# Optimization experiments

Measured on AMD Instinct MI355X. Metric: run time of the kernel, lower is better.

The kernel has to match this reference:

```python
import jax, jax.numpy as jnp
import numpy as np

N, E, F_IN, H, G, C = 50000, 600000, 128, 128, 500, 10


def _lin(k, fi, fo):
    # Glorot-ish scaled init for a [fi, fo] weight
    return (jax.random.normal(k, (fi, fo), jnp.float32) / np.float32(np.sqrt(fi)))


def setup_inputs() -> dict:
    key = jax.random.key(0)
    ks = jax.random.split(key, 16)
    x = jax.random.normal(ks[0], (N, F_IN), jnp.float32)
    edge_index = jax.random.randint(ks[1], (2, E), 0, N, dtype=jnp.int32)
    batch = jnp.sort(jax.random.randint(ks[2], (N,), 0, G, dtype=jnp.int32))
    return {
        "x": x, "edge_index": edge_index, "batch": batch,
        # SAGEConv i: out = mean_aggr @ Wl + bl + x @ Wr  (PyG default: mean aggr, root weight, bias on lin_l)
        "Wl1": _lin(ks[3], F_IN, H), "bl1": jnp.zeros((H,), jnp.float32), "Wr1": _lin(ks[4], F_IN, H),
        "Wl2": _lin(ks[5], H, H),    "bl2": jnp.zeros((H,), jnp.float32), "Wr2": _lin(ks[6], H, H),
        "Wl3": _lin(ks[7], H, H),    "bl3": jnp.zeros((H,), jnp.float32), "Wr3": _lin(ks[8], H, H),
        "W4": _lin(ks[9], H, 64), "b4": jnp.zeros((64,), jnp.float32),
        "W5": _lin(ks[10], 64, C), "b5": jnp.zeros((C,), jnp.float32),
    }


def _segment_mean(vals, ids, num_segments):
    s = jax.ops.segment_sum(vals, ids, num_segments=num_segments)
    cnt = jax.ops.segment_sum(jnp.ones((vals.shape[0], 1), vals.dtype), ids, num_segments=num_segments)
    return s / jnp.maximum(cnt, 1.0)


def _sage_conv(x, src, dst, Wl, bl, Wr):
    # gather source features along edges, mean-aggregate at destinations
    aggr = _segment_mean(x[src], dst, N)  # [N, F]
    return aggr @ Wl + bl + x @ Wr


def reference(x, edge_index, batch, Wl1, bl1, Wr1, Wl2, bl2, Wr2, Wl3, bl3, Wr3, W4, b4, W5, b5):
    src, dst = edge_index[0], edge_index[1]
    h = jax.nn.relu(_sage_conv(x, src, dst, Wl1, bl1, Wr1))
    h = jax.nn.relu(_sage_conv(h, src, dst, Wl2, bl2, Wr2))
    h = jax.nn.relu(_sage_conv(h, src, dst, Wl3, bl3, Wr3))
    g = _segment_mean(h, batch, G)          # global mean pool -> [G, H]
    g = jax.nn.relu(g @ W4 + b4)
    return jax.nn.log_softmax(g @ W5 + b5, axis=-1)
```

## Files before the change

### kernel.cpp

```cpp
#include <hip/hip_runtime.h>
#include <hip/hip_bf16.h>
#include <math.h>

#define FH 128

typedef __attribute__((ext_vector_type(8))) short short8v;
typedef __attribute__((ext_vector_type(4))) float float4v;
typedef unsigned short ushort_t;
typedef unsigned int   uint32;

__device__ __forceinline__ ushort_t f2bf(float f) {
    uint32 u = __builtin_bit_cast(uint32, f);
    u += 0x7fffu + ((u >> 16) & 1u);
    return (ushort_t)(u >> 16);
}
__device__ __forceinline__ float bf_lo(uint32 w) { return __builtin_bit_cast(float, w << 16); }
__device__ __forceinline__ float bf_hi(uint32 w) { return __builtin_bit_cast(float, w & 0xffff0000u); }
__device__ __forceinline__ uint32 pack2(float lo, float hi) {
    return (uint32)f2bf(lo) | ((uint32)f2bf(hi) << 16);
}

__device__ __forceinline__ void pack_one(const float* __restrict__ Wl,
                                         const float* __restrict__ Wr,
                                         ushort_t* __restrict__ Bp, int t) {
    int k = t >> 7, n = t & 127;
    float v = (k < FH) ? Wl[k * FH + n] : Wr[(k - FH) * FH + n];
    int nt = n >> 4, kt = k >> 5;
    int lane = (n & 15) + (((k >> 3) & 3) << 4);
    int j = k & 7;
    Bp[(((nt * 8 + kt) * 64) + lane) * 8 + j] = f2bf(v);
}

__global__ __launch_bounds__(256) void fused_prep_kernel(
        const float* __restrict__ x, ushort_t* __restrict__ xb, size_t n, int cvtBlocks,
        const float* __restrict__ Wl1, const float* __restrict__ Wr1, ushort_t* __restrict__ Bp1,
        const float* __restrict__ Wl2, const float* __restrict__ Wr2, ushort_t* __restrict__ Bp2,
        const float* __restrict__ Wl3, const float* __restrict__ Wr3, ushort_t* __restrict__ Bp3,
        const int* __restrict__ dst, int* __restrict__ deg, int E, int degBlocks,
        const int* __restrict__ batch, int* __restrict__ gstart, int N, int G) {
    int b = blockIdx.x;
    if (b < cvtBlocks) {
        size_t base = ((size_t)b * 256 + threadIdx.x) * 8;
        if (base >= n) return;
        const float4 a = *(const float4*)(x + base);
        const float4 c = *(const float4*)(x + base + 4);
        ushort_t o[8] = {f2bf(a.x), f2bf(a.y), f2bf(a.z), f2bf(a.w),
                         f2bf(c.x), f2bf(c.y), f2bf(c.z), f2bf(c.w)};
        *(uint4*)(xb + base) = *(const uint4*)o;
        return;
    }
    b -= cvtBlocks;
    if (b < 384) {
        int which = b >> 7;
        int t = (b & 127) * 256 + threadIdx.x;
        if (which == 0)      pack_one(Wl1, Wr1, Bp1, t);
        else if (which == 1) pack_one(Wl2, Wr2, Bp2, t);
        else                 pack_one(Wl3, Wr3, Bp3, t);
        return;
    }
    b -= 384;
    if (b < degBlocks) {
        int e = b * 256 + threadIdx.x;
        if (e < E) atomicAdd(&deg[dst[e]], 1);
        return;
    }
    b -= degBlocks;
    {
        int g = b * 256 + threadIdx.x;
        if (g > G) return;
        int lo = 0, hi = N;
        while (lo < hi) {
            int mid = (lo + hi) >> 1;
            if (batch[mid] < g) lo = mid + 1; else hi = mid;
        }
        gstart[g] = lo;
    }
}

__global__ __launch_bounds__(256) void scan1_kernel(const int* __restrict__ deg,
                                                    int* __restrict__ rowptr,
                                                    int* __restrict__ blockSums, int N) {
    __shared__ int lds[256];
    const int base = blockIdx.x * 1024;
    const int t = threadIdx.x;
    int v[4]; int sum = 0;
    #pragma unroll
    for (int j = 0; j < 4; ++j) {
        int idx = base + t * 4 + j;
        v[j] = (idx < N) ? deg[idx] : 0;
        sum += v[j];
    }
    lds[t] = sum; __syncthreads();
    for (int off = 1; off < 256; off <<= 1) {
        int val = lds[t];
        int add = (t >= off) ? lds[t - off] : 0;
        __syncthreads();
        lds[t] = val + add;
        __syncthreads();
    }
    int run = (t > 0) ? lds[t - 1] : 0;
    #pragma unroll
    for (int j = 0; j < 4; ++j) {
        int idx = base + t * 4 + j;
        if (idx < N) rowptr[idx] = run;
        run += v[j];
    }
    if (t == 255) blockSums[blockIdx.x] = lds[255];
}

__global__ void scan2_kernel(int* __restrict__ blockSums, int* __restrict__ rowptr,
                             int nb, int N) {
    if (threadIdx.x == 0 && blockIdx.x == 0) {
        int carry = 0;
        for (int i = 0; i < nb; ++i) {
            int s = blockSums[i];
            blockSums[i] = carry;
            carry += s;
        }
        rowptr[N] = carry;
    }
}

__global__ __launch_bounds__(256) void scan3_kernel(int* __restrict__ rowptr,
                                                    int* __restrict__ pos,
                                                    const int* __restrict__ blockSums, int N) {
    const int base = blockIdx.x * 1024;
    const int add = blockSums[blockIdx.x];
    #pragma unroll
    for (int j = 0; j < 4; ++j) {
        int idx = base + threadIdx.x * 4 + j;
        if (idx < N) {
            int v = rowptr[idx] + add;
            rowptr[idx] = v;
            pos[idx] = v;
        }
    }
}

__global__ __launch_bounds__(256) void fill_csr_kernel(const int* __restrict__ src,
                                                       const int* __restrict__ dst,
                                                       int* __restrict__ pos,
                                                       int* __restrict__ csr, int E) {
    int e = blockIdx.x * 256 + threadIdx.x;
    if (e >= E) return;
    int idx = atomicAdd(&pos[dst[e]], 1);
    csr[idx] = src[e];
}

__global__ __launch_bounds__(256) void pull_mean_kernel(const ushort_t* __restrict__ x,
                                                        const int* __restrict__ rowptr,
                                                        const int* __restrict__ csr,
                                                        ushort_t* __restrict__ aggr, int N) {
    const int v = (blockIdx.x * 256 + threadIdx.x) >> 6;
    if (v >= N) return;
    const int lane = threadIdx.x & 63;
    const int grp  = lane >> 4;
    const int li   = lane & 15;
    const int beg = rowptr[v], end = rowptr[v + 1];
    const uint4* xp = (const uint4*)x + li;

    const uint4 z = {0u, 0u, 0u, 0u};
    uint4 w0 = z, w1 = z, w2 = z, w3 = z;
    const int i0 = beg + grp;
    if (i0 < end)      w0 = xp[(size_t)csr[i0] * 16];
    if (i0 + 4 < end)  w1 = xp[(size_t)csr[i0 + 4] * 16];
    if (i0 + 8 < end)  w2 = xp[(size_t)csr[i0 + 8] * 16];
    if (i0 + 12 < end) w3 = xp[(size_t)csr[i0 + 12] * 16];

    float a0 = (bf_lo(w0.x) + bf_lo(w1.x)) + (bf_lo(w2.x) + bf_lo(w3.x));
    float a1 = (bf_hi(w0.x) + bf_hi(w1.x)) + (bf_hi(w2.x) + bf_hi(w3.x));
    float a2 = (bf_lo(w0.y) + bf_lo(w1.y)) + (bf_lo(w2.y) + bf_lo(w3.y));
    float a3 = (bf_hi(w0.y) + bf_hi(w1.y)) + (bf_hi(w2.y) + bf_hi(w3.y));
    float a4 = (bf_lo(w0.z) + bf_lo(w1.z)) + (bf_lo(w2.z) + bf_lo(w3.z));
    float a5 = (bf_hi(w0.z) + bf_hi(w1.z)) + (bf_hi(w2.z) + bf_hi(w3.z));
    float a6 = (bf_lo(w0.w) + bf_lo(w1.w)) + (bf_lo(w2.w) + bf_lo(w3.w));
    float a7 = (bf_hi(w0.w) + bf_hi(w1.w)) + (bf_hi(w2.w) + bf_hi(w3.w));

    for (int i = beg + 16 + grp; i < end; i += 4) {
        const uint4 w = xp[(size_t)csr[i] * 16];
        a0 += bf_lo(w.x); a1 += bf_hi(w.x); a2 += bf_lo(w.y); a3 += bf_hi(w.y);
        a4 += bf_lo(w.z); a5 += bf_hi(w.z); a6 += bf_lo(w.w); a7 += bf_hi(w.w);
    }

    a0 += __shfl_xor(a0, 16); a1 += __shfl_xor(a1, 16);
    a2 += __shfl_xor(a2, 16); a3 += __shfl_xor(a3, 16);
    a4 += __shfl_xor(a4, 16); a5 += __shfl_xor(a5, 16);
    a6 += __shfl_xor(a6, 16); a7 += __shfl_xor(a7, 16);
    a0 += __shfl_xor(a0, 32); a1 += __shfl_xor(a1, 32);
    a2 += __shfl_xor(a2, 32); a3 += __shfl_xor(a3, 32);
    a4 += __shfl_xor(a4, 32); a5 += __shfl_xor(a5, 32);
    a6 += __shfl_xor(a6, 32); a7 += __shfl_xor(a7, 32);

    if (grp == 0) {
        const float inv = 1.0f / (float)max(end - beg, 1);
        uint4 o;
        o.x = pack2(a0 * inv, a1 * inv);
        o.y = pack2(a2 * inv, a3 * inv);
        o.z = pack2(a4 * inv, a5 * inv);
        o.w = pack2(a6 * inv, a7 * inv);
        ((uint4*)aggr)[(size_t)v * 16 + li] = o;
    }
}

#define SO_STRIDE 136
__global__ __launch_bounds__(256) void sage_mfma_kernel(const ushort_t* __restrict__ xin,
                                                        const ushort_t* __restrict__ aggr,
                                                        const ushort_t* __restrict__ Bp,
                                                        const float* __restrict__ bl,
                                                        ushort_t* __restrict__ out, int M) {
    __shared__ ushort_t sB[32768];
    const int tid = threadIdx.x;
    {
        const uint4* s = (const uint4*)Bp;
        uint4* d = (uint4*)sB;
        #pragma unroll
        for (int i = 0; i < 16; ++i)
            d[tid + 256 * i] = s[tid + 256 * i];
    }
    __syncthreads();

    const int wave = tid >> 6;
    const int lane = tid & 63;
    const int grp  = lane >> 4;
    const int li   = lane & 15;
    const int rowBase = (blockIdx.x * 4 + wave) * 16;
    const int arow = min(rowBase + li, M - 1);

    short8v afrag[8];
    #pragma unroll
    for (int kt = 0; kt < 4; ++kt)
        afrag[kt] = *(const short8v*)(aggr + (size_t)arow * FH + kt * 32 + grp * 8);
    #pragma unroll
    for (int kt = 0; kt < 4; ++kt)
        afrag[4 + kt] = *(const short8v*)(xin + (size_t)arow * FH + kt * 32 + grp * 8);

    float4v acc[8];
    #pragma unroll
    for (int nt = 0; nt < 8; ++nt) {
        acc[nt] = (float4v){0.f, 0.f, 0.f, 0.f};
        #pragma unroll
        for (int kt = 0; kt < 8; ++kt) {
            const short8v b = *(const short8v*)(sB + (((nt * 8 + kt) * 64) + lane) * 8);
            acc[nt] = __builtin_amdgcn_mfma_f32_16x16x32_bf16(afrag[kt], b, acc[nt], 0, 0, 0);
        }
    }

    __syncthreads();

    ushort_t* so = sB + wave * (16 * SO_STRIDE);
    #pragma unroll
    for (int nt = 0; nt < 8; ++nt) {
        const float bias = bl[nt * 16 + li];
        #pragma unroll
        for (int r = 0; r < 4; ++r)
            so[(grp * 4 + r) * SO_STRIDE + nt * 16 + li] = f2bf(fmaxf(acc[nt][r] + bias, 0.f));
    }
    #pragma unroll
    for (int t = 0; t < 4; ++t) {
        const int idx = lane + 64 * t;
        const int r  = idx >> 4;
        const int ch = idx & 15;
        const int row = rowBase + r;
        if (row < M) {
            const uint4 val = *(const uint4*)(so + r * SO_STRIDE + ch * 8);
            *(uint4*)(out + (size_t)row * FH + ch * 8) = val;
        }
    }
}

__global__ __launch_bounds__(256) void head_kernel(const ushort_t* __restrict__ h,
                                                   const int* __restrict__ gstart,
                                                   const float* __restrict__ W4,
                                                   const float* __restrict__ b4,
                                                   const float* __restrict__ W5,
                                                   const float* __restrict__ b5,
                                                   float* __restrict__ out, int G) {
    __shared__ float sred[4][FH];
    __shared__ float sg2[64];
    __shared__ float sl[10];
    __shared__ float slse;
    const int g = blockIdx.x;
    const int t = threadIdx.x;
    const int wave = t >> 6, lane = t & 63;
    const int beg = gstart[g], end = gstart[g + 1];

    const uint32* hp = (const uint32*)h + lane;
    float a0 = 0.f, a1 = 0.f;
    for (int i = beg + wave; i < end; i += 4) {
        const uint32 w = hp[(size_t)i * 64];
        a0 += bf_lo(w); a1 += bf_hi(w);
    }
    sred[wave][lane * 2]     = a0;
    sred[wave][lane * 2 + 1] = a1;
    __syncthreads();
    if (t < FH) {
        const float s = sred[0][t] + sred[1][t] + sred[2][t] + sred[3][t];
        sred[0][t] = s / (float)max(end - beg, 1);
    }
    __syncthreads();
    if (t < 64) {
        float acc = b4[t];
        #pragma unroll 4
        for (int k = 0; k < FH; ++k)
            acc += sred[0][k] * W4[k * 64 + t];
        sg2[t] = fmaxf(acc, 0.f);
    }
    __syncthreads();
    if (t < 10) {
        float acc = b5[t];
        #pragma unroll 4
        for (int k = 0; k < 64; ++k)
            acc += sg2[k] * W5[k * 10 + t];
        sl[t] = acc;
    }
    __syncthreads();
    if (t == 0) {
        float m = sl[0];
        #pragma unroll
        for (int j = 1; j < 10; ++j) m = fmaxf(m, sl[j]);
        float s = 0.f;
        #pragma unroll
        for (int j = 0; j < 10; ++j) s += expf(sl[j] - m);
        slse = m + logf(s);
    }
    __syncthreads();
    if (t < 10) out[g * 10 + t] = sl[t] - slse;
}

extern "C" void kernel_launch(void* const* d_in, const int* in_sizes, int n_in,
                              void* d_out, int out_size, void* d_ws, size_t ws_size,
                              hipStream_t stream) {
    const float* x     = (const float*)d_in[0];
    const int*   ei    = (const int*)d_in[1];
    const int*   batch = (const int*)d_in[2];
    const float* Wl1 = (const float*)d_in[3];
    const float* bl1 = (const float*)d_in[4];
    const float* Wr1 = (const float*)d_in[5];
    const float* Wl2 = (const float*)d_in[6];
    const float* bl2 = (const float*)d_in[7];
    const float* Wr2 = (const float*)d_in[8];
    const float* Wl3 = (const float*)d_in[9];
    const float* bl3 = (const float*)d_in[10];
    const float* Wr3 = (const float*)d_in[11];
    const float* W4  = (const float*)d_in[12];
    const float* b4  = (const float*)d_in[13];
    const float* W5  = (const float*)d_in[14];
    const float* b5  = (const float*)d_in[15];
    float* out = (float*)d_out;

    const int N = in_sizes[0] / FH;
    const int E = in_sizes[1] / 2;
    const int G = out_size / 10;
    const int* src = ei;
    const int* dst = ei + E;

    char* p = (char*)d_ws;
    auto take = [&](size_t bytes) { char* q = p; p += (bytes + 255) & ~(size_t)255; return q; };
    ushort_t* xb    = (ushort_t*)take((size_t)N * FH * 2);
    ushort_t* h     = (ushort_t*)take((size_t)N * FH * 2);
    ushort_t* aggrb = (ushort_t*)take((size_t)N * FH * 2);
    int* deg        = (int*)take((size_t)N * 4);
    int* rowptr     = (int*)take((size_t)(N + 1) * 4);
    int* pos        = (int*)take((size_t)N * 4);
    int* csr        = (int*)take((size_t)E * 4);
    int* blockSums  = (int*)take(256 * 4);
    ushort_t* Bp1   = (ushort_t*)take(256 * FH * 2);
    ushort_t* Bp2   = (ushort_t*)take(256 * FH * 2);
    ushort_t* Bp3   = (ushort_t*)take(256 * FH * 2);
    int* gstart     = (int*)take((size_t)(G + 1) * 4);

    const int nb = (N + 1023) / 1024;

    hipMemsetAsync(deg, 0, (size_t)N * 4, stream);

    const int cvtBlocks = (int)(((size_t)N * FH / 8 + 255) / 256);
    const int degBlocks = (E + 255) / 256;
    const int gbBlocks  = (G + 1 + 255) / 256;
    fused_prep_kernel<<<cvtBlocks + 384 + degBlocks + gbBlocks, 256, 0, stream>>>(
        x, xb, (size_t)N * FH, cvtBlocks,
        Wl1, Wr1, Bp1, Wl2, Wr2, Bp2, Wl3, Wr3, Bp3,
        dst, deg, E, degBlocks,
        batch, gstart, N, G);

    scan1_kernel<<<nb, 256, 0, stream>>>(deg, rowptr, blockSums, N);
    scan2_kernel<<<1, 64, 0, stream>>>(blockSums, rowptr, nb, N);
    scan3_kernel<<<nb, 256, 0, stream>>>(rowptr, pos, blockSums, N);
    fill_csr_kernel<<<(E + 255) / 256, 256, 0, stream>>>(src, dst, pos, csr, E);

    const int pullGrid = (N * 64 + 255) / 256;
    const int gemmGrid = (N + 63) / 64;

    pull_mean_kernel<<<pullGrid, 256, 0, stream>>>(xb, rowptr, csr, aggrb, N);
    sage_mfma_kernel<<<gemmGrid, 256, 0, stream>>>(xb, aggrb, Bp1, bl1, h, N);

    pull_mean_kernel<<<pullGrid, 256, 0, stream>>>(h, rowptr, csr, aggrb, N);
    sage_mfma_kernel<<<gemmGrid, 256, 0, stream>>>(h, aggrb, Bp2, bl2, h, N);

    pull_mean_kernel<<<pullGrid, 256, 0, stream>>>(h, rowptr, csr, aggrb, N);
    sage_mfma_kernel<<<gemmGrid, 256, 0, stream>>>(h, aggrb, Bp3, bl3, h, N);

    head_kernel<<<G, 256, 0, stream>>>(h, gstart, W4, b4, W5, b5, out, G);
}
```

Baseline: 219.6 us.

## Fold block-sum scan into scan3, halve GEMM LDS, replace memset with kernel

Removes the single-thread scan2 launch: each scan3 block now computes its own prefix over the block sums with a wavefront reduction, and the last block writes the total. The SAGE GEMM loads the packed weight matrix into LDS in two halves of 32 KB instead of 64 KB, which lowers per-block LDS use and may raise occupancy, at the cost of an extra barrier. hipMemsetAsync is replaced with a small vectorized zero kernel. Together these reduce launch count and serial work, though the split weight load adds synchronization inside the GEMM.

Measured after the change: 221.4 us. No clear change (+0.8%).

```diff
diff --git a/kernel.cpp b/kernel.cpp
--- a/kernel.cpp
+++ b/kernel.cpp
@@ -18,6 +18,15 @@
 __device__ __forceinline__ float bf_hi(uint32 w) { return __builtin_bit_cast(float, w & 0xffff0000u); }
 __device__ __forceinline__ uint32 pack2(float lo, float hi) {
     return (uint32)f2bf(lo) | ((uint32)f2bf(hi) << 16);
+}
+
+__global__ __launch_bounds__(256) void zero_kernel(int* __restrict__ p, int n) {
+    int i = (blockIdx.x * 256 + threadIdx.x) * 4;
+    if (i + 3 < n) {
+        *(int4*)(p + i) = make_int4(0, 0, 0, 0);
+    } else {
+        for (int j = i; j < n; ++j) p[j] = 0;
+    }
 }
 
 __device__ __forceinline__ void pack_one(const float* __restrict__ Wl,
@@ -108,24 +117,30 @@
     if (t == 255) blockSums[blockIdx.x] = lds[255];
 }
 
-__global__ void scan2_kernel(int* __restrict__ blockSums, int* __restrict__ rowptr,
-                             int nb, int N) {
-    if (threadIdx.x == 0 && blockIdx.x == 0) {
-        int carry = 0;
-        for (int i = 0; i < nb; ++i) {
-            int s = blockSums[i];
-            blockSums[i] = carry;
-            carry += s;
-        }
-        rowptr[N] = carry;
-    }
-}
-
 __global__ __launch_bounds__(256) void scan3_kernel(int* __restrict__ rowptr,
                                                     int* __restrict__ pos,
-                                                    const int* __restrict__ blockSums, int N) {
+                                                    const int* __restrict__ blockSums,
+                                                    int N, int nb) {
+    __shared__ int sAdd, sTot;
+    if (threadIdx.x < 64) {
+        const int lane = threadIdx.x;
+        const int bid = blockIdx.x;
+        int pre = 0, tot = 0;
+        for (int i = lane; i < nb; i += 64) {
+            const int v = blockSums[i];
+            tot += v;
+            if (i < bid) pre += v;
+        }
+        #pragma unroll
+        for (int off = 1; off < 64; off <<= 1) {
+            pre += __shfl_xor(pre, off);
+            tot += __shfl_xor(tot, off);
+        }
+        if (lane == 0) { sAdd = pre; sTot = tot; }
+    }
+    __syncthreads();
+    const int add = sAdd;
     const int base = blockIdx.x * 1024;
-    const int add = blockSums[blockIdx.x];
     #pragma unroll
     for (int j = 0; j < 4; ++j) {
         int idx = base + threadIdx.x * 4 + j;
@@ -135,6 +150,7 @@
             pos[idx] = v;
         }
     }
+    if (blockIdx.x == (unsigned)(nb - 1) && threadIdx.x == 0) rowptr[N] = sTot;
 }
 
 __global__ __launch_bounds__(256) void fill_csr_kernel(const int* __restrict__ src,
@@ -208,17 +224,8 @@
                                                         const ushort_t* __restrict__ Bp,
                                                         const float* __restrict__ bl,
                                                         ushort_t* __restrict__ out, int M) {
-    __shared__ ushort_t sB[32768];
+    __shared__ ushort_t sB[16384];
     const int tid = threadIdx.x;
-    {
-        const uint4* s = (const uint4*)Bp;
-        uint4* d = (uint4*)sB;
-        #pragma unroll
-        for (int i = 0; i < 16; ++i)
-            d[tid + 256 * i] = s[tid + 256 * i];
-    }
-    __syncthreads();
-
     const int wave = tid >> 6;
     const int lane = tid & 63;
     const int grp  = lane >> 4;
@@ -236,12 +243,25 @@
 
     float4v acc[8];
     #pragma unroll
-    for (int nt = 0; nt < 8; ++nt) {
-        acc[nt] = (float4v){0.f, 0.f, 0.f, 0.f};
+    for (int ch = 0; ch < 2; ++ch) {
+        if (ch) __syncthreads();
+        {
+            const uint4* s = (const uint4*)Bp + ch * 2048;
+            uint4* d = (uint4*)sB;
+            #pragma unroll
+            for (int i = 0; i < 8; ++i)
+                d[tid + 256 * i] = s[tid + 256 * i];
+        }
+        __syncthreads();
         #pragma unroll
-        for (int kt = 0; kt < 8; ++kt) {
-            const short8v b = *(const short8v*)(sB + (((nt * 8 + kt) * 64) + lane) * 8);
-            acc[nt] = __builtin_amdgcn_mfma_f32_16x16x32_bf16(afrag[kt], b, acc[nt], 0, 0, 0);
+        for (int ntl = 0; ntl < 4; ++ntl) {
+            const int nt = ch * 4 + ntl;
+            acc[nt] = (float4v){0.f, 0.f, 0.f, 0.f};
+            #pragma unroll
+            for (int kt = 0; kt < 8; ++kt) {
+                const short8v b = *(const short8v*)(sB + (((ntl * 8 + kt) * 64) + lane) * 8);
+                acc[nt] = __builtin_amdgcn_mfma_f32_16x16x32_bf16(afrag[kt], b, acc[nt], 0, 0, 0);
+            }
         }
     }
 
@@ -371,7 +391,7 @@
 
     const int nb = (N + 1023) / 1024;
 
-    hipMemsetAsync(deg, 0, (size_t)N * 4, stream);
+    zero_kernel<<<(N / 4 + 255) / 256, 256, 0, stream>>>(deg, N);
 
     const int cvtBlocks = (int)(((size_t)N * FH / 8 + 255) / 256);
     const int degBlocks = (E + 255) / 256;
@@ -383,8 +403,7 @@
         batch, gstart, N, G);
 
     scan1_kernel<<<nb, 256, 0, stream>>>(deg, rowptr, blockSums, N);
-    scan2_kernel<<<1, 64, 0, stream>>>(blockSums, rowptr, nb, N);
-    scan3_kernel<<<nb, 256, 0, stream>>>(rowptr, pos, blockSums, N);
+    scan3_kernel<<<nb, 256, 0, stream>>>(rowptr, pos, blockSums, N, nb);
     fill_csr_kernel<<<(E + 255) / 256, 256, 0, stream>>>(src, dst, pos, csr, E);
 
     const int pullGrid = (N * 64 + 255) / 256;
```
